# Optimization experiments

Hardware: AMD Instinct MI355X
Metric: run time of the kernel (lower is better)

## Reference

```python
import jax, jax.numpy as jnp
import numpy as np

N_NODES = 50000
N_EDGES = 300000
HIDDEN = 256


def setup_inputs() -> dict:
    key = jax.random.key(0)
    k_e, k_ei, k_rev, k_w, k_b = jax.random.split(key, 5)
    E = jax.random.normal(k_e, (N_EDGES, HIDDEN), dtype=jnp.float32)
    edge_index = jax.random.randint(k_ei, (2, N_EDGES), 0, N_NODES, dtype=jnp.int64)
    rev_index = jax.random.randint(k_rev, (N_EDGES,), 0, N_EDGES, dtype=jnp.int64)
    # Linear(hidden, hidden) params, torch-style: y = x @ W.T + b
    W = jax.random.normal(k_w, (HIDDEN, HIDDEN), dtype=jnp.float32) * (1.0 / np.sqrt(HIDDEN))
    b = jax.random.normal(k_b, (HIDDEN,), dtype=jnp.float32) * 0.01
    return {"E": E, "edge_index": edge_index, "rev_index": rev_index, "W": W, "b": b}


def reference(E, edge_index, rev_index, W, b):
    src, dest = edge_index[0], edge_index[1]
    H_uv = jax.nn.relu(E)                                   # [n_edges, hidden]
    # scatter-reduce (sum) edge messages into destination nodes
    M_v = jax.ops.segment_sum(H_uv, dest, num_segments=N_NODES)  # [n_nodes, hidden]
    # gather back to edges, subtract reverse-edge message
    M_uv = M_v[src] - H_uv[rev_index]                       # [n_edges, hidden]
    # linear update (dropout p=0 is identity)
    return M_uv @ W.T + b                                   # [n_edges, hidden]
```

## Files before the change

### kernel.cpp

```cpp
#include <hip/hip_runtime.h>
#include <hip/hip_bf16.h>

typedef unsigned short ushort_t;
typedef __attribute__((ext_vector_type(8))) short short8;
typedef __attribute__((ext_vector_type(4))) float f32x4;

#define HIDDEN 256
#define N_NODES 50000
#define BM 64
#define LDSROW 512

__device__ __forceinline__ unsigned int f2bf(float f) {
    union { float f; unsigned int i; } v; v.f = f;
    return (v.i + 0x7fffu + ((v.i >> 16) & 1u)) >> 16;
}
__device__ __forceinline__ float bf2f(unsigned int u) {
    union { unsigned int i; float f; } v; v.i = u << 16; return v.f;
}

#define OFF_MVB    0u
#define OFF_WF     25600000u
#define OFF_CNT    25731072u
#define OFF_OFFS   25931072u
#define OFF_CUR    26131076u
#define OFF_ELIST  26331076u
#define OFF_BSUM   27531076u

#define SCAN_NBLK ((N_NODES + 255) / 256)

__global__ void convert_w_frag(const float* __restrict__ W, ushort_t* __restrict__ Wf, int n) {
    int i = blockIdx.x * blockDim.x + threadIdx.x;
    if (i >= n) return;
    const int t    = i & 7;
    const int lane = (i >> 3) & 63;
    const int kk   = (i >> 9) & 7;
    const int g    = i >> 12;
    const int j = g * 16 + (lane & 15);
    const int k = kk * 32 + ((lane >> 4) & 3) * 8 + t;
    Wf[i] = (ushort_t)f2bf(W[j * HIDDEN + k]);
}

__global__ void count_dst(const int* __restrict__ dst, int* __restrict__ cnt, int n) {
    int i = blockIdx.x * blockDim.x + threadIdx.x;
    if (i < n) atomicAdd(&cnt[dst[i]], 1);
}

__global__ __launch_bounds__(256)
void block_scan(const int* __restrict__ cnt, int* __restrict__ offs,
                int* __restrict__ bsum) {
    __shared__ int sh[256];
    const int t = threadIdx.x;
    const int idx = blockIdx.x * 256 + t;
    int v = (idx < N_NODES) ? cnt[idx] : 0;
    sh[t] = v;
    __syncthreads();
    for (int off = 1; off < 256; off <<= 1) {
        int x = (t >= off) ? sh[t - off] : 0;
        __syncthreads();
        sh[t] += x;
        __syncthreads();
    }
    if (idx < N_NODES) offs[idx] = sh[t] - v;
    if (t == 255) bsum[blockIdx.x] = sh[255];
}

__global__ __launch_bounds__(256)
void scan_bsum(int* __restrict__ bsum, int nb) {
    __shared__ int sh[256];
    const int t = threadIdx.x;
    int v = (t < nb) ? bsum[t] : 0;
    sh[t] = v;
    __syncthreads();
    for (int off = 1; off < 256; off <<= 1) {
        int x = (t >= off) ? sh[t - off] : 0;
        __syncthreads();
        sh[t] += x;
        __syncthreads();
    }
    if (t < nb) bsum[t] = sh[t] - v;
}

__global__ __launch_bounds__(256)
void add_base(int* __restrict__ offs, const int* __restrict__ bsum,
              int* __restrict__ cur, int n_edges) {
    const int idx = blockIdx.x * 256 + threadIdx.x;
    if (idx < N_NODES) {
        int o = offs[idx] + bsum[idx >> 8];
        offs[idx] = o;
        cur[idx] = o;
    }
    if (idx == 0) offs[N_NODES] = n_edges;
}

__global__ void fill_elist(const int* __restrict__ dst, int* __restrict__ cur,
                           int* __restrict__ elist, int n) {
    int i = blockIdx.x * blockDim.x + threadIdx.x;
    if (i < n) {
        int d = dst[i];
        int pos = atomicAdd(&cur[d], 1);
        elist[pos] = i;
    }
}

__global__ __launch_bounds__(256)
void node_gather_sum(const float* __restrict__ E,
                     const int* __restrict__ offs,
                     const int* __restrict__ elist,
                     unsigned int* __restrict__ Mvb) {
    const int w    = blockIdx.x * 4 + (threadIdx.x >> 6);
    const int node = w >> 1;
    const int half = w & 1;
    const int lane = threadIdx.x & 63;
    if (node >= N_NODES) return;
    const float* Eh = E + half * 128 + lane * 2;
    const int s0 = offs[node];
    const int s1 = offs[node + 1];
    float ax = 0.f, ay = 0.f;
    int j = s0;
    for (; j + 4 <= s1; j += 4) {
        const int e0 = elist[j], e1 = elist[j + 1], e2 = elist[j + 2], e3 = elist[j + 3];
        float2 v0 = *(const float2*)(Eh + (size_t)e0 * HIDDEN);
        float2 v1 = *(const float2*)(Eh + (size_t)e1 * HIDDEN);
        float2 v2 = *(const float2*)(Eh + (size_t)e2 * HIDDEN);
        float2 v3 = *(const float2*)(Eh + (size_t)e3 * HIDDEN);
        ax += fmaxf(v0.x, 0.f) + fmaxf(v1.x, 0.f) + fmaxf(v2.x, 0.f) + fmaxf(v3.x, 0.f);
        ay += fmaxf(v0.y, 0.f) + fmaxf(v1.y, 0.f) + fmaxf(v2.y, 0.f) + fmaxf(v3.y, 0.f);
    }
    for (; j < s1; ++j) {
        float2 v = *(const float2*)(Eh + (size_t)elist[j] * HIDDEN);
        ax += fmaxf(v.x, 0.f);
        ay += fmaxf(v.y, 0.f);
    }
    Mvb[(size_t)node * 128 + half * 64 + lane] = f2bf(ax) | (f2bf(ay) << 16);
}

__global__ __launch_bounds__(256, 3)
void gemm_fused(const float* __restrict__ E,
                const int* __restrict__ src,
                const int* __restrict__ rev,
                const unsigned int* __restrict__ Mvb,
                const ushort_t* __restrict__ Wf,
                const float* __restrict__ bias,
                float* __restrict__ out, int n_edges) {
    __shared__ __align__(16) unsigned char lds[BM * LDSROW];
    const int tid = threadIdx.x;
    const int row0 = blockIdx.x * BM;
    const int lane = tid & 63;
    const int wid  = tid >> 6;

    {
        const int wrow = wid * 16;
#pragma unroll
        for (int rr = 0; rr < 16; rr += 4) {
            float4 ev[4];
            uint2  mv[4];
            const int rbase = wrow + rr;
#pragma unroll
            for (int i = 0; i < 4; ++i) {
                int gr = row0 + rbase + i;
                int grc = (gr < n_edges) ? gr : (n_edges - 1);
                const int s  = src[grc];
                const int rv = rev[grc];
                ev[i] = *(const float4*)(E + (size_t)rv * HIDDEN + lane * 4);
                mv[i] = *(const uint2*)(Mvb + (size_t)s * (HIDDEN / 2) + lane * 2);
            }
#pragma unroll
            for (int i = 0; i < 4; ++i) {
                const int r = rbase + i;
                uint2 o;
                o.x = f2bf(bf2f(mv[i].x & 0xffffu) - fmaxf(ev[i].x, 0.f)) |
                      (f2bf(bf2f(mv[i].x >> 16)    - fmaxf(ev[i].y, 0.f)) << 16);
                o.y = f2bf(bf2f(mv[i].y & 0xffffu) - fmaxf(ev[i].z, 0.f)) |
                      (f2bf(bf2f(mv[i].y >> 16)    - fmaxf(ev[i].w, 0.f)) << 16);
                const int slot = (lane >> 1) ^ (r & 7);
                *(uint2*)(lds + r * LDSROW + slot * 16 + (lane & 1) * 8) = o;
            }
        }
    }
    __syncthreads();

    const int l15   = lane & 15;
    const int hi16  = lane >> 4;
    const int wcol0 = wid * 64;
    const int r7l   = l15 & 7;

    f32x4 acc[4][4];
#pragma unroll
    for (int m = 0; m < 4; ++m)
#pragma unroll
        for (int n = 0; n < 4; ++n)
            acc[m][n] = (f32x4){0.f, 0.f, 0.f, 0.f};

#pragma unroll 2
    for (int kk = 0; kk < 8; ++kk) {
        const int slotbyte = ((kk * 4 + hi16) ^ r7l) * 16;
        short8 a[4], bfr[4];
#pragma unroll
        for (int m = 0; m < 4; ++m)
            a[m] = *(const short8*)(lds + (m * 16 + l15) * LDSROW + slotbyte);
#pragma unroll
        for (int n = 0; n < 4; ++n)
            bfr[n] = *(const short8*)(Wf + (size_t)((((wid * 4 + n) * 8 + kk) * 64 + lane) << 3));
#pragma unroll
        for (int m = 0; m < 4; ++m)
#pragma unroll
            for (int n = 0; n < 4; ++n)
                acc[m][n] = __builtin_amdgcn_mfma_f32_16x16x32_bf16(bfr[n], a[m], acc[m][n], 0, 0, 0);
    }

#pragma unroll
    for (int m = 0; m < 4; ++m) {
        const int row = row0 + m * 16 + l15;
        if (row < n_edges) {
            float* orow = out + (size_t)row * HIDDEN;
#pragma unroll
            for (int n = 0; n < 4; ++n) {
                const int cb = wcol0 + n * 16 + hi16 * 4;
                float4 bv = *(const float4*)(bias + cb);
                float4 o;
                o.x = acc[m][n][0] + bv.x;
                o.y = acc[m][n][1] + bv.y;
                o.z = acc[m][n][2] + bv.z;
                o.w = acc[m][n][3] + bv.w;
                *(float4*)(orow + cb) = o;
            }
        }
    }
}

extern "C" void kernel_launch(void* const* d_in, const int* in_sizes, int n_in,
                              void* d_out, int out_size, void* d_ws, size_t ws_size,
                              hipStream_t stream) {
    const float* E    = (const float*)d_in[0];
    const int*   ei   = (const int*)d_in[1];
    const int*   rev  = (const int*)d_in[2];
    const float* W    = (const float*)d_in[3];
    const float* bias = (const float*)d_in[4];
    float* out = (float*)d_out;
    const int n_edges = in_sizes[2];
    const int* srcI = ei;
    const int* dstI = ei + n_edges;

    char* ws = (char*)d_ws;
    unsigned int* Mvb  = (unsigned int*)(ws + OFF_MVB);
    ushort_t*     Wf   = (ushort_t*)(ws + OFF_WF);
    int*          cnt  = (int*)(ws + OFF_CNT);
    int*          offs = (int*)(ws + OFF_OFFS);
    int*          cur  = (int*)(ws + OFF_CUR);
    int*          elst = (int*)(ws + OFF_ELIST);
    int*          bsum = (int*)(ws + OFF_BSUM);

    hipMemsetAsync(cnt, 0, N_NODES * sizeof(int), stream);

    convert_w_frag<<<(HIDDEN * HIDDEN + 255) / 256, 256, 0, stream>>>(W, Wf, HIDDEN * HIDDEN);

    count_dst<<<(n_edges + 255) / 256, 256, 0, stream>>>(dstI, cnt, n_edges);
    block_scan<<<SCAN_NBLK, 256, 0, stream>>>(cnt, offs, bsum);
    scan_bsum<<<1, 256, 0, stream>>>(bsum, SCAN_NBLK);
    add_base<<<SCAN_NBLK, 256, 0, stream>>>(offs, bsum, cur, n_edges);
    fill_elist<<<(n_edges + 255) / 256, 256, 0, stream>>>(dstI, cur, elst, n_edges);

    const int nwaves = N_NODES * 2;
    node_gather_sum<<<(nwaves + 3) / 4, 256, 0, stream>>>(E, offs, elst, Mvb);

    const int nblk = (n_edges + BM - 1) / BM;
    gemm_fused<<<nblk, 256, 0, stream>>>(E, srcI, rev, Mvb, Wf, bias, out, n_edges);
}
```

Measured before the change: 286.1 us.

## Apply linear layer before aggregation via linearity, then fuse gather-subtract-scatter per node

Uses linearity to compute P = relu(E)·W^T per edge first (stored as bf16), then sums P over incoming edges per node and writes each outgoing edge's output as node sum minus P[rev] plus bias. CSR lists are built for both destination and source adjacency so a single node kernel does the aggregation and the output writes. This removes the separate gather of relu(E) and the M_v staging, and writes outputs grouped by source node instead of in GEMM row order. In exchange it adds a 150MB bf16 intermediate, scattered output writes, and extra rounding, because the summed values are now bf16 projections rather than bf16 messages.

```diff
diff --git a/kernel.cpp b/kernel.cpp
--- a/kernel.cpp
+++ b/kernel.cpp
@@ -9,6 +9,7 @@
 #define N_NODES 50000
 #define BM 64
 #define LDSROW 512
+#define NTOT (2 * N_NODES)
 
 __device__ __forceinline__ unsigned int f2bf(float f) {
     union { float f; unsigned int i; } v; v.f = f;
@@ -18,15 +19,15 @@
     union { unsigned int i; float f; } v; v.i = u << 16; return v.f;
 }
 
-#define OFF_MVB    0u
-#define OFF_WF     25600000u
-#define OFF_CNT    25731072u
-#define OFF_OFFS   25931072u
-#define OFF_CUR    26131076u
-#define OFF_ELIST  26331076u
-#define OFF_BSUM   27531076u
-
-#define SCAN_NBLK ((N_NODES + 255) / 256)
+#define OFF_P      0u
+#define OFF_WF     153600000u
+#define OFF_CNT    153731072u
+#define OFF_OFFS   154131072u
+#define OFF_CUR    154531076u
+#define OFF_ELIST  154931076u
+#define OFF_BSUM   157331076u
+
+#define SCAN_NBLK ((NTOT + 255) / 256)
 
 __global__ void convert_w_frag(const float* __restrict__ W, ushort_t* __restrict__ Wf, int n) {
     int i = blockIdx.x * blockDim.x + threadIdx.x;
@@ -40,9 +41,18 @@
     Wf[i] = (ushort_t)f2bf(W[j * HIDDEN + k]);
 }
 
-__global__ void count_dst(const int* __restrict__ dst, int* __restrict__ cnt, int n) {
+__global__ void zero_i32(int* __restrict__ p, int n) {
     int i = blockIdx.x * blockDim.x + threadIdx.x;
-    if (i < n) atomicAdd(&cnt[dst[i]], 1);
+    if (i < n) p[i] = 0;
+}
+
+__global__ void count_both(const int* __restrict__ src, const int* __restrict__ dst,
+                           int* __restrict__ cnt, int n) {
+    int i = blockIdx.x * blockDim.x + threadIdx.x;
+    if (i < n) {
+        atomicAdd(&cnt[dst[i]], 1);
+        atomicAdd(&cnt[N_NODES + src[i]], 1);
+    }
 }
 
 __global__ __launch_bounds__(256)
@@ -51,7 +61,7 @@
     __shared__ int sh[256];
     const int t = threadIdx.x;
     const int idx = blockIdx.x * 256 + t;
-    int v = (idx < N_NODES) ? cnt[idx] : 0;
+    int v = (idx < NTOT) ? cnt[idx] : 0;
     sh[t] = v;
     __syncthreads();
     for (int off = 1; off < 256; off <<= 1) {
@@ -60,18 +70,18 @@
         sh[t] += x;
         __syncthreads();
     }
-    if (idx < N_NODES) offs[idx] = sh[t] - v;
+    if (idx < NTOT) offs[idx] = sh[t] - v;
     if (t == 255) bsum[blockIdx.x] = sh[255];
 }
 
-__global__ __launch_bounds__(256)
+__global__ __launch_bounds__(1024)
 void scan_bsum(int* __restrict__ bsum, int nb) {
-    __shared__ int sh[256];
+    __shared__ int sh[1024];
     const int t = threadIdx.x;
     int v = (t < nb) ? bsum[t] : 0;
     sh[t] = v;
     __syncthreads();
-    for (int off = 1; off < 256; off <<= 1) {
+    for (int off = 1; off < 1024; off <<= 1) {
         int x = (t >= off) ? sh[t - off] : 0;
         __syncthreads();
         sh[t] += x;
@@ -84,64 +94,29 @@
 void add_base(int* __restrict__ offs, const int* __restrict__ bsum,
               int* __restrict__ cur, int n_edges) {
     const int idx = blockIdx.x * 256 + threadIdx.x;
-    if (idx < N_NODES) {
+    if (idx < NTOT) {
         int o = offs[idx] + bsum[idx >> 8];
         offs[idx] = o;
         cur[idx] = o;
     }
-    if (idx == 0) offs[N_NODES] = n_edges;
-}
-
-__global__ void fill_elist(const int* __restrict__ dst, int* __restrict__ cur,
-                           int* __restrict__ elist, int n) {
+    if (idx == 0) offs[NTOT] = 2 * n_edges;
+}
+
+__global__ void fill_both(const int* __restrict__ src, const int* __restrict__ dst,
+                          int* __restrict__ cur, int* __restrict__ elist, int n) {
     int i = blockIdx.x * blockDim.x + threadIdx.x;
     if (i < n) {
-        int d = dst[i];
-        int pos = atomicAdd(&cur[d], 1);
-        elist[pos] = i;
-    }
-}
-
-__global__ __launch_bounds__(256)
-void node_gather_sum(const float* __restrict__ E,
-                     const int* __restrict__ offs,
-                     const int* __restrict__ elist,
-                     unsigned int* __restrict__ Mvb) {
-    const int w    = blockIdx.x * 4 + (threadIdx.x >> 6);
-    const int node = w >> 1;
-    const int half = w & 1;
-    const int lane = threadIdx.x & 63;
-    if (node >= N_NODES) return;
-    const float* Eh = E + half * 128 + lane * 2;
-    const int s0 = offs[node];
-    const int s1 = offs[node + 1];
-    float ax = 0.f, ay = 0.f;
-    int j = s0;
-    for (; j + 4 <= s1; j += 4) {
-        const int e0 = elist[j], e1 = elist[j + 1], e2 = elist[j + 2], e3 = elist[j + 3];
-        float2 v0 = *(const float2*)(Eh + (size_t)e0 * HIDDEN);
-        float2 v1 = *(const float2*)(Eh + (size_t)e1 * HIDDEN);
-        float2 v2 = *(const float2*)(Eh + (size_t)e2 * HIDDEN);
-        float2 v3 = *(const float2*)(Eh + (size_t)e3 * HIDDEN);
-        ax += fmaxf(v0.x, 0.f) + fmaxf(v1.x, 0.f) + fmaxf(v2.x, 0.f) + fmaxf(v3.x, 0.f);
-        ay += fmaxf(v0.y, 0.f) + fmaxf(v1.y, 0.f) + fmaxf(v2.y, 0.f) + fmaxf(v3.y, 0.f);
-    }
-    for (; j < s1; ++j) {
-        float2 v = *(const float2*)(Eh + (size_t)elist[j] * HIDDEN);
-        ax += fmaxf(v.x, 0.f);
-        ay += fmaxf(v.y, 0.f);
-    }
-    Mvb[(size_t)node * 128 + half * 64 + lane] = f2bf(ax) | (f2bf(ay) << 16);
-}
-
-__global__ __launch_bounds__(256, 3)
-void gemm_fused(const float* __restrict__ E,
-                const int* __restrict__ src,
-                const int* __restrict__ rev,
-                const unsigned int* __restrict__ Mvb,
-                const ushort_t* __restrict__ Wf,
-                const float* __restrict__ bias,
-                float* __restrict__ out, int n_edges) {
+        int pd = atomicAdd(&cur[dst[i]], 1);
+        elist[pd] = i;
+        int ps = atomicAdd(&cur[N_NODES + src[i]], 1);
+        elist[ps] = i;
+    }
+}
+
+__global__ __launch_bounds__(256, 4)
+void gemm_P(const float* __restrict__ E,
+            const ushort_t* __restrict__ Wf,
+            unsigned int* __restrict__ P, int n_edges) {
     __shared__ __align__(16) unsigned char lds[BM * LDSROW];
     const int tid = threadIdx.x;
     const int row0 = blockIdx.x * BM;
@@ -153,25 +128,19 @@
 #pragma unroll
         for (int rr = 0; rr < 16; rr += 4) {
             float4 ev[4];
-            uint2  mv[4];
             const int rbase = wrow + rr;
 #pragma unroll
             for (int i = 0; i < 4; ++i) {
                 int gr = row0 + rbase + i;
                 int grc = (gr < n_edges) ? gr : (n_edges - 1);
-                const int s  = src[grc];
-                const int rv = rev[grc];
-                ev[i] = *(const float4*)(E + (size_t)rv * HIDDEN + lane * 4);
-                mv[i] = *(const uint2*)(Mvb + (size_t)s * (HIDDEN / 2) + lane * 2);
+                ev[i] = *(const float4*)(E + (size_t)grc * HIDDEN + lane * 4);
             }
 #pragma unroll
             for (int i = 0; i < 4; ++i) {
                 const int r = rbase + i;
                 uint2 o;
-                o.x = f2bf(bf2f(mv[i].x & 0xffffu) - fmaxf(ev[i].x, 0.f)) |
-                      (f2bf(bf2f(mv[i].x >> 16)    - fmaxf(ev[i].y, 0.f)) << 16);
-                o.y = f2bf(bf2f(mv[i].y & 0xffffu) - fmaxf(ev[i].z, 0.f)) |
-                      (f2bf(bf2f(mv[i].y >> 16)    - fmaxf(ev[i].w, 0.f)) << 16);
+                o.x = f2bf(fmaxf(ev[i].x, 0.f)) | (f2bf(fmaxf(ev[i].y, 0.f)) << 16);
+                o.y = f2bf(fmaxf(ev[i].z, 0.f)) | (f2bf(fmaxf(ev[i].w, 0.f)) << 16);
                 const int slot = (lane >> 1) ^ (r & 7);
                 *(uint2*)(lds + r * LDSROW + slot * 16 + (lane & 1) * 8) = o;
             }
@@ -212,19 +181,85 @@
     for (int m = 0; m < 4; ++m) {
         const int row = row0 + m * 16 + l15;
         if (row < n_edges) {
-            float* orow = out + (size_t)row * HIDDEN;
+            unsigned int* prow = P + (size_t)row * (HIDDEN / 2);
 #pragma unroll
             for (int n = 0; n < 4; ++n) {
                 const int cb = wcol0 + n * 16 + hi16 * 4;
-                float4 bv = *(const float4*)(bias + cb);
-                float4 o;
-                o.x = acc[m][n][0] + bv.x;
-                o.y = acc[m][n][1] + bv.y;
-                o.z = acc[m][n][2] + bv.z;
-                o.w = acc[m][n][3] + bv.w;
-                *(float4*)(orow + cb) = o;
+                uint2 o;
+                o.x = f2bf(acc[m][n][0]) | (f2bf(acc[m][n][1]) << 16);
+                o.y = f2bf(acc[m][n][2]) | (f2bf(acc[m][n][3]) << 16);
+                *(uint2*)(prow + (cb >> 1)) = o;
             }
         }
+    }
+}
+
+__global__ __launch_bounds__(256)
+void node_fused(const unsigned int* __restrict__ P,
+                const int* __restrict__ offs,
+                const int* __restrict__ elist,
+                const int* __restrict__ rev,
+                const float* __restrict__ bias,
+                float* __restrict__ out) {
+    const int node = blockIdx.x * 4 + (threadIdx.x >> 6);
+    const int lane = threadIdx.x & 63;
+    if (node >= N_NODES) return;
+
+    const int d0 = offs[node];
+    const int d1 = offs[node + 1];
+    float q0 = 0.f, q1 = 0.f, q2 = 0.f, q3 = 0.f;
+    int j = d0;
+    for (; j + 4 <= d1; j += 4) {
+        const int e0 = elist[j], e1 = elist[j + 1], e2 = elist[j + 2], e3 = elist[j + 3];
+        uint2 p0 = *(const uint2*)(P + (size_t)e0 * (HIDDEN / 2) + lane * 2);
+        uint2 p1 = *(const uint2*)(P + (size_t)e1 * (HIDDEN / 2) + lane * 2);
+        uint2 p2 = *(const uint2*)(P + (size_t)e2 * (HIDDEN / 2) + lane * 2);
+        uint2 p3 = *(const uint2*)(P + (size_t)e3 * (HIDDEN / 2) + lane * 2);
+        q0 += bf2f(p0.x & 0xffffu) + bf2f(p1.x & 0xffffu) + bf2f(p2.x & 0xffffu) + bf2f(p3.x & 0xffffu);
+        q1 += bf2f(p0.x >> 16)     + bf2f(p1.x >> 16)     + bf2f(p2.x >> 16)     + bf2f(p3.x >> 16);
+        q2 += bf2f(p0.y & 0xffffu) + bf2f(p1.y & 0xffffu) + bf2f(p2.y & 0xffffu) + bf2f(p3.y & 0xffffu);
+        q3 += bf2f(p0.y >> 16)     + bf2f(p1.y >> 16)     + bf2f(p2.y >> 16)     + bf2f(p3.y >> 16);
+    }
+    for (; j < d1; ++j) {
+        uint2 p = *(const uint2*)(P + (size_t)elist[j] * (HIDDEN / 2) + lane * 2);
+        q0 += bf2f(p.x & 0xffffu);
+        q1 += bf2f(p.x >> 16);
+        q2 += bf2f(p.y & 0xffffu);
+        q3 += bf2f(p.y >> 16);
+    }
+    float4 bv = *(const float4*)(bias + lane * 4);
+    q0 += bv.x; q1 += bv.y; q2 += bv.z; q3 += bv.w;
+
+    const int s0 = offs[N_NODES + node];
+    const int s1 = offs[N_NODES + node + 1];
+    j = s0;
+    for (; j + 2 <= s1; j += 2) {
+        const int e0 = elist[j], e1 = elist[j + 1];
+        const int r0 = rev[e0], r1 = rev[e1];
+        uint2 p0 = *(const uint2*)(P + (size_t)r0 * (HIDDEN / 2) + lane * 2);
+        uint2 p1 = *(const uint2*)(P + (size_t)r1 * (HIDDEN / 2) + lane * 2);
+        float4 o0, o1;
+        o0.x = q0 - bf2f(p0.x & 0xffffu);
+        o0.y = q1 - bf2f(p0.x >> 16);
+        o0.z = q2 - bf2f(p0.y & 0xffffu);
+        o0.w = q3 - bf2f(p0.y >> 16);
+        o1.x = q0 - bf2f(p1.x & 0xffffu);
+        o1.y = q1 - bf2f(p1.x >> 16);
+        o1.z = q2 - bf2f(p1.y & 0xffffu);
+        o1.w = q3 - bf2f(p1.y >> 16);
+        *(float4*)(out + (size_t)e0 * HIDDEN + lane * 4) = o0;
+        *(float4*)(out + (size_t)e1 * HIDDEN + lane * 4) = o1;
+    }
+    for (; j < s1; ++j) {
+        const int e = elist[j];
+        const int r = rev[e];
+        uint2 p = *(const uint2*)(P + (size_t)r * (HIDDEN / 2) + lane * 2);
+        float4 o;
+        o.x = q0 - bf2f(p.x & 0xffffu);
+        o.y = q1 - bf2f(p.x >> 16);
+        o.z = q2 - bf2f(p.y & 0xffffu);
+        o.w = q3 - bf2f(p.y >> 16);
+        *(float4*)(out + (size_t)e * HIDDEN + lane * 4) = o;
     }
 }
 
@@ -242,7 +277,7 @@
     const int* dstI = ei + n_edges;
 
     char* ws = (char*)d_ws;
-    unsigned int* Mvb  = (unsigned int*)(ws + OFF_MVB);
+    unsigned int* P    = (unsigned int*)(ws + OFF_P);
     ushort_t*     Wf   = (ushort_t*)(ws + OFF_WF);
     int*          cnt  = (int*)(ws + OFF_CNT);
     int*          offs = (int*)(ws + OFF_OFFS);
@@ -250,19 +285,17 @@
     int*          elst = (int*)(ws + OFF_ELIST);
     int*          bsum = (int*)(ws + OFF_BSUM);
 
-    hipMemsetAsync(cnt, 0, N_NODES * sizeof(int), stream);
-
+    zero_i32<<<SCAN_NBLK, 256, 0, stream>>>(cnt, NTOT);
     convert_w_frag<<<(HIDDEN * HIDDEN + 255) / 256, 256, 0, stream>>>(W, Wf, HIDDEN * HIDDEN);
 
-    count_dst<<<(n_edges + 255) / 256, 256, 0, stream>>>(dstI, cnt, n_edges);
+    count_both<<<(n_edges + 255) / 256, 256, 0, stream>>>(srcI, dstI, cnt, n_edges);
     block_scan<<<SCAN_NBLK, 256, 0, stream>>>(cnt, offs, bsum);
-    scan_bsum<<<1, 256, 0, stream>>>(bsum, SCAN_NBLK);
+    scan_bsum<<<1, 1024, 0, stream>>>(bsum, SCAN_NBLK);
     add_base<<<SCAN_NBLK, 256, 0, stream>>>(offs, bsum, cur, n_edges);
-    fill_elist<<<(n_edges + 255) / 256, 256, 0, stream>>>(dstI, cur, elst, n_edges);
-
-    const int nwaves = N_NODES * 2;
-    node_gather_sum<<<(nwaves + 3) / 4, 256, 0, stream>>>(E, offs, elst, Mvb);
+    fill_both<<<(n_edges + 255) / 256, 256, 0, stream>>>(srcI, dstI, cur, elst, n_edges);
 
     const int nblk = (n_edges + BM - 1) / BM;
-    gemm_fused<<<nblk, 256, 0, stream>>>(E, srcI, rev, Mvb, Wf, bias, out, n_edges);
-}
+    gemm_P<<<nblk, 256, 0, stream>>>(E, Wf, P, n_edges);
+
+    node_fused<<<(N_NODES + 3) / 4, 256, 0, stream>>>(P, offs, elst, rev, bias, out);
+}
```

After: 331.7 us. 15.9% more time.

## Emit bf16 relu(E) copy during node gather and read it in GEMM

Applied to the files above, without the earlier changes.

The node-gather kernel now writes a bf16-packed relu(E) row for each edge it visits. The fused GEMM gathers the reverse-edge rows from this half-size buffer instead of fp32 E, which cuts random-gather bytes. Occupancy hint for the GEMM rises and its gather loop batches 8 rows; the memset is replaced by a zero kernel. It adds a large scattered write and extra bf16 rounding of relu(E) before subtraction.

```diff
diff --git a/kernel.cpp b/kernel.cpp
--- a/kernel.cpp
+++ b/kernel.cpp
@@ -25,6 +25,7 @@
 #define OFF_CUR    26131076u
 #define OFF_ELIST  26331076u
 #define OFF_BSUM   27531076u
+#define OFF_EB     27540000u
 
 #define SCAN_NBLK ((N_NODES + 255) / 256)
 
@@ -38,6 +39,11 @@
     const int j = g * 16 + (lane & 15);
     const int k = kk * 32 + ((lane >> 4) & 3) * 8 + t;
     Wf[i] = (ushort_t)f2bf(W[j * HIDDEN + k]);
+}
+
+__global__ void zero_i32(int* __restrict__ p, int n) {
+    int i = blockIdx.x * blockDim.x + threadIdx.x;
+    if (i < n) p[i] = 0;
 }
 
 __global__ void count_dst(const int* __restrict__ dst, int* __restrict__ cnt, int n) {
@@ -106,13 +112,15 @@
 void node_gather_sum(const float* __restrict__ E,
                      const int* __restrict__ offs,
                      const int* __restrict__ elist,
-                     unsigned int* __restrict__ Mvb) {
+                     unsigned int* __restrict__ Mvb,
+                     unsigned int* __restrict__ Eb) {
     const int w    = blockIdx.x * 4 + (threadIdx.x >> 6);
     const int node = w >> 1;
     const int half = w & 1;
     const int lane = threadIdx.x & 63;
     if (node >= N_NODES) return;
     const float* Eh = E + half * 128 + lane * 2;
+    unsigned int* Ebh = Eb + half * 64 + lane;
     const int s0 = offs[node];
     const int s1 = offs[node + 1];
     float ax = 0.f, ay = 0.f;
@@ -123,19 +131,30 @@
         float2 v1 = *(const float2*)(Eh + (size_t)e1 * HIDDEN);
         float2 v2 = *(const float2*)(Eh + (size_t)e2 * HIDDEN);
         float2 v3 = *(const float2*)(Eh + (size_t)e3 * HIDDEN);
-        ax += fmaxf(v0.x, 0.f) + fmaxf(v1.x, 0.f) + fmaxf(v2.x, 0.f) + fmaxf(v3.x, 0.f);
-        ay += fmaxf(v0.y, 0.f) + fmaxf(v1.y, 0.f) + fmaxf(v2.y, 0.f) + fmaxf(v3.y, 0.f);
+        float r0x = fmaxf(v0.x, 0.f), r0y = fmaxf(v0.y, 0.f);
+        float r1x = fmaxf(v1.x, 0.f), r1y = fmaxf(v1.y, 0.f);
+        float r2x = fmaxf(v2.x, 0.f), r2y = fmaxf(v2.y, 0.f);
+        float r3x = fmaxf(v3.x, 0.f), r3y = fmaxf(v3.y, 0.f);
+        ax += r0x + r1x + r2x + r3x;
+        ay += r0y + r1y + r2y + r3y;
+        Ebh[(size_t)e0 * 128] = f2bf(r0x) | (f2bf(r0y) << 16);
+        Ebh[(size_t)e1 * 128] = f2bf(r1x) | (f2bf(r1y) << 16);
+        Ebh[(size_t)e2 * 128] = f2bf(r2x) | (f2bf(r2y) << 16);
+        Ebh[(size_t)e3 * 128] = f2bf(r3x) | (f2bf(r3y) << 16);
     }
     for (; j < s1; ++j) {
-        float2 v = *(const float2*)(Eh + (size_t)elist[j] * HIDDEN);
-        ax += fmaxf(v.x, 0.f);
-        ay += fmaxf(v.y, 0.f);
+        const int e = elist[j];
+        float2 v = *(const float2*)(Eh + (size_t)e * HIDDEN);
+        float rx = fmaxf(v.x, 0.f), ry = fmaxf(v.y, 0.f);
+        ax += rx;
+        ay += ry;
+        Ebh[(size_t)e * 128] = f2bf(rx) | (f2bf(ry) << 16);
     }
     Mvb[(size_t)node * 128 + half * 64 + lane] = f2bf(ax) | (f2bf(ay) << 16);
 }
 
-__global__ __launch_bounds__(256, 3)
-void gemm_fused(const float* __restrict__ E,
+__global__ __launch_bounds__(256, 5)
+void gemm_fused(const unsigned int* __restrict__ Eb,
                 const int* __restrict__ src,
                 const int* __restrict__ rev,
                 const unsigned int* __restrict__ Mvb,
@@ -151,27 +170,25 @@
     {
         const int wrow = wid * 16;
 #pragma unroll
-        for (int rr = 0; rr < 16; rr += 4) {
-            float4 ev[4];
-            uint2  mv[4];
-            const int rbase = wrow + rr;
-#pragma unroll
-            for (int i = 0; i < 4; ++i) {
-                int gr = row0 + rbase + i;
+        for (int rr = 0; rr < 16; rr += 8) {
+            uint2 eb[8], mv[8];
+#pragma unroll
+            for (int i = 0; i < 8; ++i) {
+                int gr = row0 + wrow + rr + i;
                 int grc = (gr < n_edges) ? gr : (n_edges - 1);
                 const int s  = src[grc];
                 const int rv = rev[grc];
-                ev[i] = *(const float4*)(E + (size_t)rv * HIDDEN + lane * 4);
-                mv[i] = *(const uint2*)(Mvb + (size_t)s * (HIDDEN / 2) + lane * 2);
+                eb[i] = *(const uint2*)(Eb + (size_t)rv * 128 + lane * 2);
+                mv[i] = *(const uint2*)(Mvb + (size_t)s * 128 + lane * 2);
             }
 #pragma unroll
-            for (int i = 0; i < 4; ++i) {
-                const int r = rbase + i;
+            for (int i = 0; i < 8; ++i) {
+                const int r = wrow + rr + i;
                 uint2 o;
-                o.x = f2bf(bf2f(mv[i].x & 0xffffu) - fmaxf(ev[i].x, 0.f)) |
-                      (f2bf(bf2f(mv[i].x >> 16)    - fmaxf(ev[i].y, 0.f)) << 16);
-                o.y = f2bf(bf2f(mv[i].y & 0xffffu) - fmaxf(ev[i].z, 0.f)) |
-                      (f2bf(bf2f(mv[i].y >> 16)    - fmaxf(ev[i].w, 0.f)) << 16);
+                o.x = f2bf(bf2f(mv[i].x & 0xffffu) - bf2f(eb[i].x & 0xffffu)) |
+                      (f2bf(bf2f(mv[i].x >> 16)    - bf2f(eb[i].x >> 16)) << 16);
+                o.y = f2bf(bf2f(mv[i].y & 0xffffu) - bf2f(eb[i].y & 0xffffu)) |
+                      (f2bf(bf2f(mv[i].y >> 16)    - bf2f(eb[i].y >> 16)) << 16);
                 const int slot = (lane >> 1) ^ (r & 7);
                 *(uint2*)(lds + r * LDSROW + slot * 16 + (lane & 1) * 8) = o;
             }
@@ -249,9 +266,9 @@
     int*          cur  = (int*)(ws + OFF_CUR);
     int*          elst = (int*)(ws + OFF_ELIST);
     int*          bsum = (int*)(ws + OFF_BSUM);
-
-    hipMemsetAsync(cnt, 0, N_NODES * sizeof(int), stream);
-
+    unsigned int* Eb   = (unsigned int*)(ws + OFF_EB);
+
+    zero_i32<<<SCAN_NBLK, 256, 0, stream>>>(cnt, N_NODES);
     convert_w_frag<<<(HIDDEN * HIDDEN + 255) / 256, 256, 0, stream>>>(W, Wf, HIDDEN * HIDDEN);
 
     count_dst<<<(n_edges + 255) / 256, 256, 0, stream>>>(dstI, cnt, n_edges);
@@ -261,8 +278,8 @@
     fill_elist<<<(n_edges + 255) / 256, 256, 0, stream>>>(dstI, cur, elst, n_edges);
 
     const int nwaves = N_NODES * 2;
-    node_gather_sum<<<(nwaves + 3) / 4, 256, 0, stream>>>(E, offs, elst, Mvb);
+    node_gather_sum<<<(nwaves + 3) / 4, 256, 0, stream>>>(E, offs, elst, Mvb, Eb);
 
     const int nblk = (n_edges + BM - 1) / BM;
-    gemm_fused<<<nblk, 256, 0, stream>>>(E, srcI, rev, Mvb, Wf, bias, out, n_edges);
-}
+    gemm_fused<<<nblk, 256, 0, stream>>>(Eb, srcI, rev, Mvb, Wf, bias, out, n_edges);
+}
```

After: 362.1 us. +26.6%, slower.

## Split gather into two halves overlapping second-half loads with first-half MFMA

Applied to the files above, without the earlier changes.

The fused GEMM now gathers and builds the A tile in two 32-row halves. The E loads for the second half are issued before the first half's MFMA loop, and its Mvb loads and conversion follow that loop, so gather latency overlaps tensor-core work. Because the second half lands in its own LDS region, the same 32 KB LDS is used but there is an extra barrier and the W fragments are reloaded for each half. Separately, hipMemsetAsync is replaced with a small zeroing kernel to cut API/launch overhead.

```diff
diff --git a/kernel.cpp b/kernel.cpp
--- a/kernel.cpp
+++ b/kernel.cpp
@@ -8,7 +8,6 @@
 #define HIDDEN 256
 #define N_NODES 50000
 #define BM 64
-#define LDSROW 512
 
 __device__ __forceinline__ unsigned int f2bf(float f) {
     union { float f; unsigned int i; } v; v.f = f;
@@ -38,6 +37,11 @@
     const int j = g * 16 + (lane & 15);
     const int k = kk * 32 + ((lane >> 4) & 3) * 8 + t;
     Wf[i] = (ushort_t)f2bf(W[j * HIDDEN + k]);
+}
+
+__global__ void zero_i32(int* __restrict__ p, int n) {
+    int i = blockIdx.x * blockDim.x + threadIdx.x;
+    if (i < n) p[i] = 0;
 }
 
 __global__ void count_dst(const int* __restrict__ dst, int* __restrict__ cnt, int n) {
@@ -142,43 +146,11 @@
                 const ushort_t* __restrict__ Wf,
                 const float* __restrict__ bias,
                 float* __restrict__ out, int n_edges) {
-    __shared__ __align__(16) unsigned char lds[BM * LDSROW];
+    __shared__ __align__(16) unsigned char lds[2 * 32 * 512];
     const int tid = threadIdx.x;
     const int row0 = blockIdx.x * BM;
     const int lane = tid & 63;
     const int wid  = tid >> 6;
-
-    {
-        const int wrow = wid * 16;
-#pragma unroll
-        for (int rr = 0; rr < 16; rr += 4) {
-            float4 ev[4];
-            uint2  mv[4];
-            const int rbase = wrow + rr;
-#pragma unroll
-            for (int i = 0; i < 4; ++i) {
-                int gr = row0 + rbase + i;
-                int grc = (gr < n_edges) ? gr : (n_edges - 1);
-                const int s  = src[grc];
-                const int rv = rev[grc];
-                ev[i] = *(const float4*)(E + (size_t)rv * HIDDEN + lane * 4);
-                mv[i] = *(const uint2*)(Mvb + (size_t)s * (HIDDEN / 2) + lane * 2);
-            }
-#pragma unroll
-            for (int i = 0; i < 4; ++i) {
-                const int r = rbase + i;
-                uint2 o;
-                o.x = f2bf(bf2f(mv[i].x & 0xffffu) - fmaxf(ev[i].x, 0.f)) |
-                      (f2bf(bf2f(mv[i].x >> 16)    - fmaxf(ev[i].y, 0.f)) << 16);
-                o.y = f2bf(bf2f(mv[i].y & 0xffffu) - fmaxf(ev[i].z, 0.f)) |
-                      (f2bf(bf2f(mv[i].y >> 16)    - fmaxf(ev[i].w, 0.f)) << 16);
-                const int slot = (lane >> 1) ^ (r & 7);
-                *(uint2*)(lds + r * LDSROW + slot * 16 + (lane & 1) * 8) = o;
-            }
-        }
-    }
-    __syncthreads();
-
     const int l15   = lane & 15;
     const int hi16  = lane >> 4;
     const int wcol0 = wid * 64;
@@ -191,21 +163,88 @@
         for (int n = 0; n < 4; ++n)
             acc[m][n] = (f32x4){0.f, 0.f, 0.f, 0.f};
 
-#pragma unroll 2
+    {
+        float4 ev[8];
+        uint2  mv[8];
+#pragma unroll
+        for (int i = 0; i < 8; ++i) {
+            int gr = row0 + wid * 8 + i;
+            int grc = (gr < n_edges) ? gr : (n_edges - 1);
+            ev[i] = *(const float4*)(E + (size_t)rev[grc] * HIDDEN + lane * 4);
+            mv[i] = *(const uint2*)(Mvb + (size_t)src[grc] * 128 + lane * 2);
+        }
+#pragma unroll
+        for (int i = 0; i < 8; ++i) {
+            const int r = wid * 8 + i;
+            uint2 o;
+            o.x = f2bf(bf2f(mv[i].x & 0xffffu) - fmaxf(ev[i].x, 0.f)) |
+                  (f2bf(bf2f(mv[i].x >> 16)    - fmaxf(ev[i].y, 0.f)) << 16);
+            o.y = f2bf(bf2f(mv[i].y & 0xffffu) - fmaxf(ev[i].z, 0.f)) |
+                  (f2bf(bf2f(mv[i].y >> 16)    - fmaxf(ev[i].w, 0.f)) << 16);
+            const int slot = (lane >> 1) ^ (r & 7);
+            *(uint2*)(lds + r * 512 + slot * 16 + (lane & 1) * 8) = o;
+        }
+    }
+    __syncthreads();
+
+    float4 ev1[8];
+    int grc1[8];
+#pragma unroll
+    for (int i = 0; i < 8; ++i) {
+        int gr = row0 + 32 + wid * 8 + i;
+        grc1[i] = (gr < n_edges) ? gr : (n_edges - 1);
+        ev1[i] = *(const float4*)(E + (size_t)rev[grc1[i]] * HIDDEN + lane * 4);
+    }
+
+#pragma unroll
     for (int kk = 0; kk < 8; ++kk) {
         const int slotbyte = ((kk * 4 + hi16) ^ r7l) * 16;
-        short8 a[4], bfr[4];
-#pragma unroll
-        for (int m = 0; m < 4; ++m)
-            a[m] = *(const short8*)(lds + (m * 16 + l15) * LDSROW + slotbyte);
+        short8 a0, a1, bfr[4];
+        a0 = *(const short8*)(lds + (l15)      * 512 + slotbyte);
+        a1 = *(const short8*)(lds + (16 + l15) * 512 + slotbyte);
 #pragma unroll
         for (int n = 0; n < 4; ++n)
             bfr[n] = *(const short8*)(Wf + (size_t)((((wid * 4 + n) * 8 + kk) * 64 + lane) << 3));
 #pragma unroll
-        for (int m = 0; m < 4; ++m)
-#pragma unroll
-            for (int n = 0; n < 4; ++n)
-                acc[m][n] = __builtin_amdgcn_mfma_f32_16x16x32_bf16(bfr[n], a[m], acc[m][n], 0, 0, 0);
+        for (int n = 0; n < 4; ++n) {
+            acc[0][n] = __builtin_amdgcn_mfma_f32_16x16x32_bf16(bfr[n], a0, acc[0][n], 0, 0, 0);
+            acc[1][n] = __builtin_amdgcn_mfma_f32_16x16x32_bf16(bfr[n], a1, acc[1][n], 0, 0, 0);
+        }
+    }
+
+    {
+        uint2 mv[8];
+#pragma unroll
+        for (int i = 0; i < 8; ++i)
+            mv[i] = *(const uint2*)(Mvb + (size_t)src[grc1[i]] * 128 + lane * 2);
+#pragma unroll
+        for (int i = 0; i < 8; ++i) {
+            const int r = 32 + wid * 8 + i;
+            uint2 o;
+            o.x = f2bf(bf2f(mv[i].x & 0xffffu) - fmaxf(ev1[i].x, 0.f)) |
+                  (f2bf(bf2f(mv[i].x >> 16)    - fmaxf(ev1[i].y, 0.f)) << 16);
+            o.y = f2bf(bf2f(mv[i].y & 0xffffu) - fmaxf(ev1[i].z, 0.f)) |
+                  (f2bf(bf2f(mv[i].y >> 16)    - fmaxf(ev1[i].w, 0.f)) << 16);
+            const int slot = (lane >> 1) ^ (r & 7);
+            *(uint2*)(lds + 16384 + (r & 31) * 512 + slot * 16 + (lane & 1) * 8) = o;
+        }
+    }
+    __syncthreads();
+
+#pragma unroll
+    for (int kk = 0; kk < 8; ++kk) {
+        const int slotbyte = ((kk * 4 + hi16) ^ r7l) * 16;
+        short8 a2, a3, bfr[4];
+        a2 = *(const short8*)(lds + 16384 + (l15)      * 512 + slotbyte);
+        a3 = *(const short8*)(lds + 16384 + (16 + l15) * 512 + slotbyte);
+#pragma unroll
+        for (int n = 0; n < 4; ++n)
+            bfr[n] = *(const short8*)(Wf + (size_t)((((wid * 4 + n) * 8 + kk) * 64 + lane) << 3));
+#pragma unroll
+        for (int n = 0; n < 4; ++n) {
+            acc[2][n] = __builtin_amdgcn_mfma_f32_16x16x32_bf16(bfr[n], a2, acc[2][n], 0, 0, 0);
+            acc[3][n] = __builtin_amdgcn_mfma_f32_16x16x32_bf16(bfr[n], a3, acc[3][n], 0, 0, 0);
+        }
     }
 
 #pragma unroll
@@ -250,8 +289,7 @@
     int*          elst = (int*)(ws + OFF_ELIST);
     int*          bsum = (int*)(ws + OFF_BSUM);
 
-    hipMemsetAsync(cnt, 0, N_NODES * sizeof(int), stream);
-
+    zero_i32<<<SCAN_NBLK, 256, 0, stream>>>(cnt, N_NODES);
     convert_w_frag<<<(HIDDEN * HIDDEN + 255) / 256, 256, 0, stream>>>(W, Wf, HIDDEN * HIDDEN);
 
     count_dst<<<(n_edges + 255) / 256, 256, 0, stream>>>(dstI, cnt, n_edges);
```

Measured after the change: 312.4 us. 9.2% more time.
